# Kernel tuning notes

Hardware: AMD Instinct MI355X
Metric: run time of the kernel (lower is better)

The kernel has to match this reference:

```python
import jax, jax.numpy as jnp
import numpy as np

B, T, H, L, O = 256, 512, 512, 2, 2

def setup_inputs() -> dict:
    key = jax.random.key(0)
    ks = jax.random.split(key, 9)
    s = 0.05
    return {
        "x": jax.random.normal(ks[0], (B, T), jnp.float32),
        # input-side gate weights, layer 0 (input dim 1); gate order: [r, z, n]
        "Wi0": jax.random.normal(ks[1], (3, H, 1), jnp.float32) * s,
        "bi0": jax.random.normal(ks[2], (3, H), jnp.float32) * s,
        # input-side gate weights, layers 1..L-1 (input dim H)
        "Wi_rest": jax.random.normal(ks[3], (L - 1, 3, H, H), jnp.float32) * s,
        "bi_rest": jax.random.normal(ks[4], (L - 1, 3, H), jnp.float32) * s,
        # hidden-side gate weights for all layers
        "Wh": jax.random.normal(ks[5], (L, 3, H, H), jnp.float32) * s,
        "bh": jax.random.normal(ks[6], (L, 3, H), jnp.float32) * s,
        "fc_w": jax.random.normal(ks[7], (O, H), jnp.float32) * s,
        "fc_b": jax.random.normal(ks[8], (O,), jnp.float32) * s,
    }


def reference(x, Wi0, bi0, Wi_rest, bi_rest, Wh, bh, fc_w, fc_b):
    nL = Wh.shape[0]
    hsz = Wh.shape[-1]
    bsz = x.shape[0]

    def step(h, x_t):  # h: [L, B, H], x_t: [B]
        inp = x_t[:, None]  # [B, 1]
        new_h = []
        for l in range(nL):
            # fuse the 3 input-side and 3 hidden-side gate GEMMs into one einsum each
            if l == 0:
                gi = jnp.einsum('bi,ghi->gbh', inp, Wi0) + bi0[:, None, :]
            else:
                gi = jnp.einsum('bi,ghi->gbh', inp, Wi_rest[l - 1]) + bi_rest[l - 1, :, None, :]
            gh = jnp.einsum('bi,ghi->gbh', h[l], Wh[l]) + bh[l, :, None, :]
            r = jax.nn.sigmoid(gi[0] + gh[0])
            z = jax.nn.sigmoid(gi[1] + gh[1])
            n = jnp.tanh(gi[2] + r * gh[2])
            hl = (1.0 - z) * n + z * h[l]
            new_h.append(hl)
            inp = hl
        return jnp.stack(new_h), None

    h0 = jnp.zeros((nL, bsz, hsz), x.dtype)
    h_final, _ = jax.lax.scan(step, h0, x.T)  # scan over time axis
    return h_final[-1] @ fc_w.T + fc_b  # [B, O]
```

## Files before the change

kernel.cpp:

```cpp
#include <hip/hip_runtime.h>


#define TLEN 512
#define HDIM 512
#define MROW 32
#define NL0  8
#define GRID 192
#define U0   64
#define U1   32
#define SLOTD (MROW*HDIM)
#define ROWB 1040
#define DEPTH 4

#define RT_BAR 10000000ULL

typedef __attribute__((ext_vector_type(8))) short bf16x8;
typedef __attribute__((ext_vector_type(4))) float f32x4;

#define AT_LD64(p)   __hip_atomic_load((const unsigned long long*)(p), __ATOMIC_RELAXED, __HIP_MEMORY_SCOPE_AGENT)
#define AT_LD32(p)   __hip_atomic_load((const unsigned*)(p), __ATOMIC_RELAXED, __HIP_MEMORY_SCOPE_AGENT)
#define AT_ST32(p,v) __hip_atomic_store((unsigned*)(p), (v), __ATOMIC_RELAXED, __HIP_MEMORY_SCOPE_AGENT)
#define AT_ST32F(p,v) __hip_atomic_store((float*)(p), (v), __ATOMIC_RELAXED, __HIP_MEMORY_SCOPE_AGENT)

__device__ __forceinline__ unsigned short f2bf(float f){
  unsigned u = __builtin_bit_cast(unsigned, f);
  u = (u + 0x7FFFu + ((u>>16)&1u)) >> 16;
  return (unsigned short)u;
}
__device__ __forceinline__ float sigm(float v){ return __builtin_amdgcn_rcpf(1.f + __expf(-v)); }
__device__ __forceinline__ float tanh_f(float v){ return 1.f - 2.f*__builtin_amdgcn_rcpf(__expf(2.f*v)+1.f); }

__device__ __forceinline__ bool wait_f1(unsigned* fl, int tB, int* sab){
  if (threadIdx.x < 64){
    const int lane = threadIdx.x;
    const int tgt = (lane<16) ? tB : (int)0x80000000;
    const unsigned long long t0 = __builtin_amdgcn_s_memrealtime();
    int ab = 0;
    for(;;){
      int f = (lane<16) ? (int)AT_LD32(fl + lane*16) : 0x7fffffff;
      if (__ballot(f >= tgt) == ~0ULL) break;
      if (__builtin_amdgcn_s_memrealtime() - t0 > RT_BAR){ ab = 1; break; }
      __builtin_amdgcn_s_sleep(1);
    }
    if (lane==0) *sab = ab;
  }
  __syncthreads();
  __builtin_amdgcn_sched_barrier(0);
  return *sab != 0;
}

__device__ __forceinline__ void stageV(const unsigned* src, unsigned short* shDst,
                                       int tid, unsigned ep, int* sab){
  const unsigned long long epat =
      ((unsigned long long)ep << 16) | ((unsigned long long)ep << 48);
  const unsigned long long emask = 0xFFFF0000FFFF0000ULL;
  unsigned long long hb[32];
  const unsigned long long t0 = __builtin_amdgcn_s_memrealtime();
  for(;;){
    #pragma unroll
    for (int i=0;i<32;++i)
      hb[i] = AT_LD64((const char*)src + tid*8 + i*2048);
    unsigned long long bad = 0;
    #pragma unroll
    for (int i=0;i<32;++i) bad |= (hb[i] ^ epat) & emask;
    if (!bad) break;
    if (__builtin_amdgcn_s_memrealtime() - t0 > RT_BAR){ *sab = 1; break; }
  }
  #pragma unroll
  for (int i=0;i<32;++i){
    unsigned v = (unsigned)(hb[i] & 0xFFFFu) | ((unsigned)((hb[i]>>32)&0xFFFFu) << 16);
    *(unsigned*)((char*)shDst + i*ROWB + tid*4) = v;
  }
}

__device__ __forceinline__ void zeroSh(unsigned short* shDst, int tid){
  #pragma unroll
  for (int i=0;i<32;++i)
    *(unsigned*)((char*)shDst + i*ROWB + tid*4) = 0u;
}

extern "C" __global__ void __launch_bounds__(256,1)
gru_persistent(const float* __restrict__ x,
               const float* __restrict__ Wi0,
               const float* __restrict__ bi0,
               const float* __restrict__ Wi1,
               const float* __restrict__ bi1,
               const float* __restrict__ Wh,
               const float* __restrict__ bh,
               const float* __restrict__ fcw,
               const float* __restrict__ fcb,
               float* __restrict__ out,
               unsigned* __restrict__ flg,
               unsigned* __restrict__ h0g,
               unsigned* __restrict__ h1g,
               float* __restrict__ h1f)
{
  __shared__ unsigned short shA[MROW*(ROWB/2)];
  __shared__ unsigned short shB[MROW*(ROWB/2)];
  __shared__ float shG[MROW*192];
  __shared__ int s_ab;

  const int tid  = threadIdx.x;
  const int lane = tid & 63;
  const int w    = tid >> 6;
  const int grp  = blockIdx.x & 7;
  const int wgid = blockIdx.x >> 3;
  const int g32  = grp*32;

  if (tid==0) s_ab = 0;
  __syncthreads();

  unsigned* fl = flg + grp*256;
  unsigned* h0 = h0g + grp*DEPTH*SLOTD;
  unsigned* h1 = h1g + grp*DEPTH*SLOTD;

  if (wgid < NL0){
    const int u0  = wgid*U0;
    const int ua2 = w*16 + (lane&15);

    bf16x8 bfr[3][16];
    #pragma unroll
    for (int nt=0; nt<3; ++nt){
      const float* wrow = Wh + (size_t)(nt*HDIM + u0 + ua2)*HDIM;
      #pragma unroll
      for (int ks=0; ks<16; ++ks){
        int k = ks*32 + (lane>>4)*8;
        const float4 f0 = *(const float4*)(wrow + k);
        const float4 f1 = *(const float4*)(wrow + k + 4);
        bf16x8 v;
        v[0]=(short)f2bf(f0.x); v[1]=(short)f2bf(f0.y); v[2]=(short)f2bf(f0.z); v[3]=(short)f2bf(f0.w);
        v[4]=(short)f2bf(f1.x); v[5]=(short)f2bf(f1.y); v[6]=(short)f2bf(f1.z); v[7]=(short)f2bf(f1.w);
        bfr[nt][ks]=v;
      }
    }
    float wi0v[3], bi0v[3], bh0v[3];
    #pragma unroll
    for (int g=0; g<3; ++g){
      wi0v[g] = Wi0[g*HDIM + u0+ua2];
      bi0v[g] = bi0[g*HDIM + u0+ua2];
      bh0v[g] = bh [g*HDIM + u0+ua2];
    }
    float h_own[8];
    #pragma unroll
    for (int j=0;j<8;++j) h_own[j]=0.f;

    for (int s=0; s<TLEN; ++s){
      float xv[2][4];
      #pragma unroll
      for (int mt=0; mt<2; ++mt)
        #pragma unroll
        for (int j=0;j<4;++j)
          xv[mt][j] = x[(g32 + mt*16 + (lane>>4)*4 + j)*TLEN + s];

      if (wait_f1(fl, s-3, &s_ab)) return;

      if (s==0) zeroSh(shA, tid);
      else      stageV(h0 + ((s-1)&3)*SLOTD, shA, tid, (unsigned)s, &s_ab);
      __syncthreads();
      if (s_ab) return;

      f32x4 acc[2][3] = {};
      #pragma unroll
      for (int ks=0; ks<16; ++ks){
        int koff = ks*64 + (lane>>4)*16;
        bf16x8 a0 = *(const bf16x8*)((const char*)shA + (lane&15)*ROWB + koff);
        bf16x8 a1 = *(const bf16x8*)((const char*)shA + ((lane&15)+16)*ROWB + koff);
        #pragma unroll
        for (int nt=0; nt<3; ++nt){
          acc[0][nt] = __builtin_amdgcn_mfma_f32_16x16x32_bf16(a0, bfr[nt][ks], acc[0][nt],0,0,0);
          acc[1][nt] = __builtin_amdgcn_mfma_f32_16x16x32_bf16(a1, bfr[nt][ks], acc[1][nt],0,0,0);
        }
      }
      unsigned* dst32 = h0 + (s&3)*SLOTD;
      const unsigned epw = (unsigned)(s+1) << 16;
      #pragma unroll
      for (int mt=0; mt<2; ++mt)
        #pragma unroll
        for (int j=0;j<4;++j){
          int b = mt*16 + (lane>>4)*4 + j;
          float G0 = acc[mt][0][j] + bh0v[0];
          float G1 = acc[mt][1][j] + bh0v[1];
          float G2 = acc[mt][2][j] + bh0v[2];
          float xvv = xv[mt][j];
          float r_ = sigm(fmaf(xvv, wi0v[0], bi0v[0]) + G0);
          float z_ = sigm(fmaf(xvv, wi0v[1], bi0v[1]) + G1);
          float n_ = tanh_f(fmaf(xvv, wi0v[2], bi0v[2]) + r_*G2);
          float hn = (1.f - z_)*n_ + z_*h_own[mt*4+j];
          h_own[mt*4+j] = hn;
          AT_ST32(dst32 + b*HDIM + u0 + ua2, epw | (unsigned)f2bf(hn));
        }
    }
    if (wgid==0){
      if (wait_f1(fl, TLEN, &s_ab)) return;
      int p = tid>>2, kl = tid&3;
      int b = p>>1, o = p&1;
      const char* h8 = (const char*)(h1f + (size_t)(g32+b)*HDIM + kl*128);
      const float2* w2 = (const float2*)(fcw + o*HDIM + kl*128);
      float a2 = 0.f;
      #pragma unroll
      for (int k=0;k<64;++k){
        unsigned long long v = AT_LD64(h8 + k*8);
        float2 hv = __builtin_bit_cast(float2, v);
        float2 wv = w2[k];
        a2 = fmaf(hv.x, wv.x, fmaf(hv.y, wv.y, a2));
      }
      a2 += __shfl_xor(a2, 1);
      a2 += __shfl_xor(a2, 2);
      if (kl==0) out[(g32+b)*2 + o] = a2 + fcb[o];
    }
  } else {
    const int wg1  = wgid - NL0;
    const int u1   = wg1*U1;
    const int colb = (w<2) ? w*48 : 96 + (w-2)*48;

    bf16x8 bfr[3][16];
    #pragma unroll
    for (int nt=0; nt<3; ++nt){
      int col = colb + nt*16 + (lane&15);
      const float* wrow;
      if (w < 2){ int g = col>>5, uu = col&31;
        wrow = Wi1 + (size_t)(g*HDIM + u1 + uu)*HDIM;
      } else {    int c2 = col-96; int g = c2>>5, uu = c2&31;
        wrow = Wh + (size_t)((3+g)*HDIM + u1 + uu)*HDIM;
      }
      #pragma unroll
      for (int ks=0; ks<16; ++ks){
        int k = ks*32 + (lane>>4)*8;
        const float4 f0 = *(const float4*)(wrow + k);
        const float4 f1 = *(const float4*)(wrow + k + 4);
        bf16x8 v;
        v[0]=(short)f2bf(f0.x); v[1]=(short)f2bf(f0.y); v[2]=(short)f2bf(f0.z); v[3]=(short)f2bf(f0.w);
        v[4]=(short)f2bf(f1.x); v[5]=(short)f2bf(f1.y); v[6]=(short)f2bf(f1.z); v[7]=(short)f2bf(f1.w);
        bfr[nt][ks]=v;
      }
    }
    const int ua   = tid & 31;
    const int brow = (tid>>5)*4;
    float bi1v[3], bh1v[3];
    #pragma unroll
    for (int g=0; g<3; ++g){
      bi1v[g] = bi1[g*HDIM + u1+ua];
      bh1v[g] = bh [(3+g)*HDIM + u1+ua];
    }
    float h_own[4];
    #pragma unroll
    for (int j=0;j<4;++j) h_own[j]=0.f;

    for (int t=1; t<=TLEN; ++t){
      stageV(h0 + ((t-1)&3)*SLOTD, shA, tid, (unsigned)t, &s_ab);
      if (t==1) zeroSh(shB, tid);
      else      stageV(h1 + ((t-2)&3)*SLOTD, shB, tid, (unsigned)(t-1), &s_ab);
      __syncthreads();
      if (s_ab) return;
      if (tid==0 && t<TLEN) AT_ST32(fl + wg1*16, (unsigned)t);

      const char* shSrc = (w<2) ? (const char*)shA : (const char*)shB;
      f32x4 acc[2][3] = {};
      #pragma unroll
      for (int ks=0; ks<16; ++ks){
        int koff = ks*64 + (lane>>4)*16;
        bf16x8 a0 = *(const bf16x8*)(shSrc + (lane&15)*ROWB + koff);
        bf16x8 a1 = *(const bf16x8*)(shSrc + ((lane&15)+16)*ROWB + koff);
        #pragma unroll
        for (int nt=0; nt<3; ++nt){
          acc[0][nt] = __builtin_amdgcn_mfma_f32_16x16x32_bf16(a0, bfr[nt][ks], acc[0][nt],0,0,0);
          acc[1][nt] = __builtin_amdgcn_mfma_f32_16x16x32_bf16(a1, bfr[nt][ks], acc[1][nt],0,0,0);
        }
      }
      #pragma unroll
      for (int mt=0; mt<2; ++mt)
        #pragma unroll
        for (int nt=0; nt<3; ++nt)
          #pragma unroll
          for (int j=0;j<4;++j){
            int b = mt*16 + (lane>>4)*4 + j;
            shG[b*192 + colb + nt*16 + (lane&15)] = acc[mt][nt][j];
          }
      __syncthreads();
      unsigned* dst32 = h1 + ((t-1)&3)*SLOTD;
      const unsigned epw = (unsigned)t << 16;
      #pragma unroll
      for (int j=0;j<4;++j){
        int b = brow + j;
        float gi0 = shG[b*192 + ua]        + bi1v[0];
        float gi1 = shG[b*192 + 32 + ua]   + bi1v[1];
        float gi2 = shG[b*192 + 64 + ua]   + bi1v[2];
        float gh0 = shG[b*192 + 96 + ua]   + bh1v[0];
        float gh1 = shG[b*192 + 128 + ua]  + bh1v[1];
        float gh2 = shG[b*192 + 160 + ua]  + bh1v[2];
        float r_ = sigm(gi0+gh0);
        float z_ = sigm(gi1+gh1);
        float n_ = tanh_f(gi2 + r_*gh2);
        float hn = (1.f - z_)*n_ + z_*h_own[j];
        h_own[j] = hn;
        AT_ST32(dst32 + b*HDIM + u1 + ua, epw | (unsigned)f2bf(hn));
        if (t == TLEN) AT_ST32F(&h1f[(size_t)(g32+b)*HDIM + u1 + ua], hn);
      }
    }
    asm volatile("s_waitcnt vmcnt(0)" ::: "memory");
    __syncthreads();
    if (tid==0) AT_ST32(fl + wg1*16, (unsigned)TLEN);
  }
}

extern "C" void kernel_launch(void* const* d_in, const int* in_sizes, int n_in,
                              void* d_out, int out_size, void* d_ws, size_t ws_size,
                              hipStream_t stream)
{
  const float* x   = (const float*)d_in[0];
  const float* Wi0 = (const float*)d_in[1];
  const float* bi0 = (const float*)d_in[2];
  const float* Wi1 = (const float*)d_in[3];
  const float* bi1 = (const float*)d_in[4];
  const float* Wh  = (const float*)d_in[5];
  const float* bh  = (const float*)d_in[6];
  const float* fcw = (const float*)d_in[7];
  const float* fcb = (const float*)d_in[8];
  float* out = (float*)d_out;

  unsigned* flg = (unsigned*)d_ws;
  unsigned* h0g = (unsigned*)((char*)d_ws + 16384);
  unsigned* h1g = (unsigned*)((char*)d_ws + 16384 + 2097152);
  float*    h1f = (float*)((char*)d_ws + 16384 + 2*2097152);

  hipMemsetAsync(d_ws, 0, 16384 + 2*2097152 + 524288, stream);
  gru_persistent<<<GRID, 256, 0, stream>>>(x,Wi0,bi0,Wi1,bi1,Wh,bh,fcw,fcb,out,
                                           flg,h0g,h1g,h1f);
}
```

Before: 2.386 ms.

## Replace epoch-tagged hidden-state polling with per-step flags and direct MFMA operand loads

The hidden state was stored as 32-bit words carrying an epoch tag, and each consumer spun on the data itself before copying it into shared memory. This change stores plain bf16 values and has every workgroup publish a per-step completion flag after a vmcnt drain and barrier. Consumers wait on layer-0 and layer-1 flags together, then load MFMA A operands straight from global memory into registers, which removes the shared-memory staging and halves the buffer size. In exchange, each step adds an explicit store drain, a barrier and a flag store, and all groups now contend on a wider flag poll.

Result: slower. 4.616 ms (+93.5%).

```diff
diff --git a/kernel.cpp b/kernel.cpp
--- a/kernel.cpp
+++ b/kernel.cpp
@@ -8,17 +8,18 @@
 #define GRID 192
 #define U0   64
 #define U1   32
-#define SLOTD (MROW*HDIM)
-#define ROWB 1040
+#define HSZE (MROW*HDIM)
 #define DEPTH 4
 
 #define RT_BAR 10000000ULL
 
 typedef __attribute__((ext_vector_type(8))) short bf16x8;
 typedef __attribute__((ext_vector_type(4))) float f32x4;
+typedef __attribute__((ext_vector_type(2))) unsigned long long u64x2;
 
 #define AT_LD64(p)   __hip_atomic_load((const unsigned long long*)(p), __ATOMIC_RELAXED, __HIP_MEMORY_SCOPE_AGENT)
 #define AT_LD32(p)   __hip_atomic_load((const unsigned*)(p), __ATOMIC_RELAXED, __HIP_MEMORY_SCOPE_AGENT)
+#define AT_ST16(p,v) __hip_atomic_store((unsigned short*)(p), (v), __ATOMIC_RELAXED, __HIP_MEMORY_SCOPE_AGENT)
 #define AT_ST32(p,v) __hip_atomic_store((unsigned*)(p), (v), __ATOMIC_RELAXED, __HIP_MEMORY_SCOPE_AGENT)
 #define AT_ST32F(p,v) __hip_atomic_store((float*)(p), (v), __ATOMIC_RELAXED, __HIP_MEMORY_SCOPE_AGENT)
 
@@ -30,14 +31,14 @@
 __device__ __forceinline__ float sigm(float v){ return __builtin_amdgcn_rcpf(1.f + __expf(-v)); }
 __device__ __forceinline__ float tanh_f(float v){ return 1.f - 2.f*__builtin_amdgcn_rcpf(__expf(2.f*v)+1.f); }
 
-__device__ __forceinline__ bool wait_f1(unsigned* fl, int tB, int* sab){
+__device__ __forceinline__ bool wait_flags(unsigned* fl, int tA, int tB, int* sab){
   if (threadIdx.x < 64){
     const int lane = threadIdx.x;
-    const int tgt = (lane<16) ? tB : (int)0x80000000;
+    const int tgt = (lane<8) ? tA : (lane<24 ? tB : (int)0x80000000);
     const unsigned long long t0 = __builtin_amdgcn_s_memrealtime();
     int ab = 0;
     for(;;){
-      int f = (lane<16) ? (int)AT_LD32(fl + lane*16) : 0x7fffffff;
+      int f = (lane<24) ? (int)AT_LD32(fl + lane*16) : 0x7fffffff;
       if (__ballot(f >= tgt) == ~0ULL) break;
       if (__builtin_amdgcn_s_memrealtime() - t0 > RT_BAR){ ab = 1; break; }
       __builtin_amdgcn_s_sleep(1);
@@ -47,36 +48,6 @@
   __syncthreads();
   __builtin_amdgcn_sched_barrier(0);
   return *sab != 0;
-}
-
-__device__ __forceinline__ void stageV(const unsigned* src, unsigned short* shDst,
-                                       int tid, unsigned ep, int* sab){
-  const unsigned long long epat =
-      ((unsigned long long)ep << 16) | ((unsigned long long)ep << 48);
-  const unsigned long long emask = 0xFFFF0000FFFF0000ULL;
-  unsigned long long hb[32];
-  const unsigned long long t0 = __builtin_amdgcn_s_memrealtime();
-  for(;;){
-    #pragma unroll
-    for (int i=0;i<32;++i)
-      hb[i] = AT_LD64((const char*)src + tid*8 + i*2048);
-    unsigned long long bad = 0;
-    #pragma unroll
-    for (int i=0;i<32;++i) bad |= (hb[i] ^ epat) & emask;
-    if (!bad) break;
-    if (__builtin_amdgcn_s_memrealtime() - t0 > RT_BAR){ *sab = 1; break; }
-  }
-  #pragma unroll
-  for (int i=0;i<32;++i){
-    unsigned v = (unsigned)(hb[i] & 0xFFFFu) | ((unsigned)((hb[i]>>32)&0xFFFFu) << 16);
-    *(unsigned*)((char*)shDst + i*ROWB + tid*4) = v;
-  }
-}
-
-__device__ __forceinline__ void zeroSh(unsigned short* shDst, int tid){
-  #pragma unroll
-  for (int i=0;i<32;++i)
-    *(unsigned*)((char*)shDst + i*ROWB + tid*4) = 0u;
 }
 
 extern "C" __global__ void __launch_bounds__(256,1)
@@ -91,12 +62,10 @@
                const float* __restrict__ fcb,
                float* __restrict__ out,
                unsigned* __restrict__ flg,
-               unsigned* __restrict__ h0g,
-               unsigned* __restrict__ h1g,
+               unsigned short* __restrict__ h0g,
+               unsigned short* __restrict__ h1g,
                float* __restrict__ h1f)
 {
-  __shared__ unsigned short shA[MROW*(ROWB/2)];
-  __shared__ unsigned short shB[MROW*(ROWB/2)];
   __shared__ float shG[MROW*192];
   __shared__ int s_ab;
 
@@ -107,12 +76,12 @@
   const int wgid = blockIdx.x >> 3;
   const int g32  = grp*32;
 
-  if (tid==0) s_ab = 0;
-  __syncthreads();
-
-  unsigned* fl = flg + grp*256;
-  unsigned* h0 = h0g + grp*DEPTH*SLOTD;
-  unsigned* h1 = h1g + grp*DEPTH*SLOTD;
+  unsigned* fl = flg + grp*512;
+  unsigned short* h0 = h0g + grp*DEPTH*HSZE;
+  unsigned short* h1 = h1g + grp*DEPTH*HSZE;
+
+  const int r0 = lane & 15;
+  const int cb = (lane>>4)*16;
 
   if (wgid < NL0){
     const int u0  = wgid*U0;
@@ -152,27 +121,33 @@
         for (int j=0;j<4;++j)
           xv[mt][j] = x[(g32 + mt*16 + (lane>>4)*4 + j)*TLEN + s];
 
-      if (wait_f1(fl, s-3, &s_ab)) return;
-
-      if (s==0) zeroSh(shA, tid);
-      else      stageV(h0 + ((s-1)&3)*SLOTD, shA, tid, (unsigned)s, &s_ab);
-      __syncthreads();
-      if (s_ab) return;
-
+      if (wait_flags(fl, s, s-3, &s_ab)) return;
+
+      const char* src = (const char*)(h0 + ((s-1)&3)*HSZE);
+      unsigned long long hb[64];
+      #pragma unroll
+      for (int ks=0; ks<16; ++ks){
+        const char* p0 = src + r0*1024 + ks*64 + cb;
+        const char* p1 = p0 + 16*1024;
+        hb[ks*4+0] = AT_LD64(p0);
+        hb[ks*4+1] = AT_LD64(p0+8);
+        hb[ks*4+2] = AT_LD64(p1);
+        hb[ks*4+3] = AT_LD64(p1+8);
+      }
       f32x4 acc[2][3] = {};
       #pragma unroll
       for (int ks=0; ks<16; ++ks){
-        int koff = ks*64 + (lane>>4)*16;
-        bf16x8 a0 = *(const bf16x8*)((const char*)shA + (lane&15)*ROWB + koff);
-        bf16x8 a1 = *(const bf16x8*)((const char*)shA + ((lane&15)+16)*ROWB + koff);
+        u64x2 t0; t0[0]=hb[ks*4+0]; t0[1]=hb[ks*4+1];
+        u64x2 t1; t1[0]=hb[ks*4+2]; t1[1]=hb[ks*4+3];
+        bf16x8 a0 = __builtin_bit_cast(bf16x8, t0);
+        bf16x8 a1 = __builtin_bit_cast(bf16x8, t1);
         #pragma unroll
         for (int nt=0; nt<3; ++nt){
           acc[0][nt] = __builtin_amdgcn_mfma_f32_16x16x32_bf16(a0, bfr[nt][ks], acc[0][nt],0,0,0);
           acc[1][nt] = __builtin_amdgcn_mfma_f32_16x16x32_bf16(a1, bfr[nt][ks], acc[1][nt],0,0,0);
         }
       }
-      unsigned* dst32 = h0 + (s&3)*SLOTD;
-      const unsigned epw = (unsigned)(s+1) << 16;
+      unsigned short* dst = h0 + (s&3)*HSZE;
       #pragma unroll
       for (int mt=0; mt<2; ++mt)
         #pragma unroll
@@ -187,11 +162,14 @@
           float n_ = tanh_f(fmaf(xvv, wi0v[2], bi0v[2]) + r_*G2);
           float hn = (1.f - z_)*n_ + z_*h_own[mt*4+j];
           h_own[mt*4+j] = hn;
-          AT_ST32(dst32 + b*HDIM + u0 + ua2, epw | (unsigned)f2bf(hn));
+          AT_ST16(&dst[b*HDIM + u0 + ua2], f2bf(hn));
         }
+      asm volatile("s_waitcnt vmcnt(0)" ::: "memory");
+      __syncthreads();
+      if (tid==0) AT_ST32(fl + wgid*16, (unsigned)(s+1));
     }
     if (wgid==0){
-      if (wait_f1(fl, TLEN, &s_ab)) return;
+      if (wait_flags(fl, (int)0x80000000, TLEN, &s_ab)) return;
       int p = tid>>2, kl = tid&3;
       int b = p>>1, o = p&1;
       const char* h8 = (const char*)(h1f + (size_t)(g32+b)*HDIM + kl*128);
@@ -209,8 +187,7 @@
       if (kl==0) out[(g32+b)*2 + o] = a2 + fcb[o];
     }
   } else {
-    const int wg1  = wgid - NL0;
-    const int u1   = wg1*U1;
+    const int u1   = (wgid-NL0)*U1;
     const int colb = (w<2) ? w*48 : 96 + (w-2)*48;
 
     bf16x8 bfr[3][16];
@@ -247,20 +224,27 @@
     for (int j=0;j<4;++j) h_own[j]=0.f;
 
     for (int t=1; t<=TLEN; ++t){
-      stageV(h0 + ((t-1)&3)*SLOTD, shA, tid, (unsigned)t, &s_ab);
-      if (t==1) zeroSh(shB, tid);
-      else      stageV(h1 + ((t-2)&3)*SLOTD, shB, tid, (unsigned)(t-1), &s_ab);
-      __syncthreads();
-      if (s_ab) return;
-      if (tid==0 && t<TLEN) AT_ST32(fl + wg1*16, (unsigned)t);
-
-      const char* shSrc = (w<2) ? (const char*)shA : (const char*)shB;
+      if (wait_flags(fl, t, t-1, &s_ab)) return;
+
+      const char* srcW = (w<2) ? (const char*)(h0 + ((t-1)&3)*HSZE)
+                               : (const char*)(h1 + ((t-2)&3)*HSZE);
+      unsigned long long hb[64];
+      #pragma unroll
+      for (int ks=0; ks<16; ++ks){
+        const char* p0 = srcW + r0*1024 + ks*64 + cb;
+        const char* p1 = p0 + 16*1024;
+        hb[ks*4+0] = AT_LD64(p0);
+        hb[ks*4+1] = AT_LD64(p0+8);
+        hb[ks*4+2] = AT_LD64(p1);
+        hb[ks*4+3] = AT_LD64(p1+8);
+      }
       f32x4 acc[2][3] = {};
       #pragma unroll
       for (int ks=0; ks<16; ++ks){
-        int koff = ks*64 + (lane>>4)*16;
-        bf16x8 a0 = *(const bf16x8*)(shSrc + (lane&15)*ROWB + koff);
-        bf16x8 a1 = *(const bf16x8*)(shSrc + ((lane&15)+16)*ROWB + koff);
+        u64x2 t0; t0[0]=hb[ks*4+0]; t0[1]=hb[ks*4+1];
+        u64x2 t1; t1[0]=hb[ks*4+2]; t1[1]=hb[ks*4+3];
+        bf16x8 a0 = __builtin_bit_cast(bf16x8, t0);
+        bf16x8 a1 = __builtin_bit_cast(bf16x8, t1);
         #pragma unroll
         for (int nt=0; nt<3; ++nt){
           acc[0][nt] = __builtin_amdgcn_mfma_f32_16x16x32_bf16(a0, bfr[nt][ks], acc[0][nt],0,0,0);
@@ -277,8 +261,7 @@
             shG[b*192 + colb + nt*16 + (lane&15)] = acc[mt][nt][j];
           }
       __syncthreads();
-      unsigned* dst32 = h1 + ((t-1)&3)*SLOTD;
-      const unsigned epw = (unsigned)t << 16;
+      unsigned short* dstB = h1 + ((t-1)&3)*HSZE;
       #pragma unroll
       for (int j=0;j<4;++j){
         int b = brow + j;
@@ -293,13 +276,13 @@
         float n_ = tanh_f(gi2 + r_*gh2);
         float hn = (1.f - z_)*n_ + z_*h_own[j];
         h_own[j] = hn;
-        AT_ST32(dst32 + b*HDIM + u1 + ua, epw | (unsigned)f2bf(hn));
+        AT_ST16(&dstB[b*HDIM + u1 + ua], f2bf(hn));
         if (t == TLEN) AT_ST32F(&h1f[(size_t)(g32+b)*HDIM + u1 + ua], hn);
       }
-    }
-    asm volatile("s_waitcnt vmcnt(0)" ::: "memory");
-    __syncthreads();
-    if (tid==0) AT_ST32(fl + wg1*16, (unsigned)TLEN);
+      asm volatile("s_waitcnt vmcnt(0)" ::: "memory");
+      __syncthreads();
+      if (tid==0) AT_ST32(fl + wgid*16, (unsigned)t);
+    }
   }
 }
 
@@ -318,12 +301,12 @@
   const float* fcb = (const float*)d_in[8];
   float* out = (float*)d_out;
 
-  unsigned* flg = (unsigned*)d_ws;
-  unsigned* h0g = (unsigned*)((char*)d_ws + 16384);
-  unsigned* h1g = (unsigned*)((char*)d_ws + 16384 + 2097152);
-  float*    h1f = (float*)((char*)d_ws + 16384 + 2*2097152);
-
-  hipMemsetAsync(d_ws, 0, 16384 + 2*2097152 + 524288, stream);
+  unsigned*       flg = (unsigned*)d_ws;
+  unsigned short* h0g = (unsigned short*)((char*)d_ws + 16384);
+  unsigned short* h1g = (unsigned short*)((char*)d_ws + 16384 + 1048576);
+  float*          h1f = (float*)((char*)d_ws + 16384 + 2*1048576);
+
+  hipMemsetAsync(d_ws, 0, 16384 + 2*1048576 + 524288, stream);
   gru_persistent<<<GRID, 256, 0, stream>>>(x,Wi0,bi0,Wi1,bi1,Wh,bh,fcw,fcb,out,
                                            flg,h0g,h1g,h1f);
 }
```
